# Optimization experiments

Hardware: AMD Instinct MI355X
Metric: run time of the kernel (lower is better)

## Reference

```python
import jax, jax.numpy as jnp
import numpy as np

B, S, DM, H, DK, R, THETA = 8, 2048, 512, 8, 64, 128, 10000.0
BLK = R          # key/query block size; window radius == block size
NB = S // BLK    # number of blocks
NEG = -1e30      # additive mask for invalid positions (fp32-safe)


def setup_inputs() -> dict:
    key = jax.random.key(0)
    ks = jax.random.split(key, 5)
    scale = 0.02
    hidden_states = jax.random.normal(ks[0], (B, S, DM), jnp.float32)
    Wq = jax.random.normal(ks[1], (DM, H * DK), jnp.float32) * scale
    Wk = jax.random.normal(ks[2], (DM, H * DK), jnp.float32) * scale
    Wv = jax.random.normal(ks[3], (DM, H * DK), jnp.float32) * scale
    Wo = jax.random.normal(ks[4], (H * DK, DM), jnp.float32) * scale
    position_ids = jnp.tile(jnp.arange(S, dtype=jnp.int64)[None, :], (B, 1))
    return {"hidden_states": hidden_states, "Wq": Wq, "Wk": Wk, "Wv": Wv,
            "Wo": Wo, "position_ids": position_ids}


def _apply_rope(q, k, position_ids):
    # q,k: [B,H,S,DK]; position_ids: [B,S]
    half = DK // 2
    inv_freq = 1.0 / (THETA ** (jnp.arange(0, DK, 2, dtype=jnp.float32) / DK))  # [half]
    freqs = position_ids.astype(jnp.float32)[:, :, None] * inv_freq[None, None, :]  # [B,S,half]
    emb = jnp.concatenate([freqs, freqs], axis=-1)        # [B,S,DK]
    cos = jnp.cos(emb)[:, None, :, :]                     # [B,1,S,DK]
    sin = jnp.sin(emb)[:, None, :, :]

    def rotate_half(x):
        return jnp.concatenate([-x[..., half:], x[..., :half]], axis=-1)

    return q * cos + rotate_half(q) * sin, k * cos + rotate_half(k) * sin


def _band_mask():
    # valid[nb, BLK, 3*BLK]: key within [0,S) and |j - i| <= R
    b = jnp.arange(NB)[:, None, None]
    qi = jnp.arange(BLK)[None, :, None]
    kj = jnp.arange(3 * BLK)[None, None, :]
    kglob = (b - 1) * BLK + kj                 # global key index
    qglob = b * BLK + qi                        # global query index
    return (jnp.abs(kglob - qglob) <= R) & (kglob >= 0) & (kglob < S)


def reference(hidden_states, Wq, Wk, Wv, Wo, position_ids):
    # projections: [B,S,DM] -> [B,H,S,DK]
    def shape(x):
        return x.reshape(B, S, H, DK).transpose(0, 2, 1, 3)

    q = shape(hidden_states @ Wq)
    k = shape(hidden_states @ Wk)
    v = shape(hidden_states @ Wv)
    q, k = _apply_rope(q, k, position_ids)

    # block-banded sliding-window attention, softmax_scale = 1.0 (no scaling)
    pad = ((0, 0), (0, 0), (BLK, BLK), (0, 0))
    kb = jnp.pad(k, pad).reshape(B, H, NB + 2, BLK, DK)
    vb = jnp.pad(v, pad).reshape(B, H, NB + 2, BLK, DK)
    # neighbor window: blocks [b-1, b, b+1] -> [B,H,NB,3*BLK,DK]
    kwin = jnp.concatenate([kb[:, :, i:i + NB] for i in range(3)], axis=3)
    vwin = jnp.concatenate([vb[:, :, i:i + NB] for i in range(3)], axis=3)
    qb = q.reshape(B, H, NB, BLK, DK)

    scores = jnp.einsum('bhnqd,bhnkd->bhnqk', qb, kwin)   # unscaled
    valid = _band_mask()                                  # [NB,BLK,3*BLK]
    scores = jnp.where(valid[None, None], scores, NEG)
    attn = jax.nn.softmax(scores.astype(jnp.float32), axis=-1).astype(scores.dtype)
    outb = jnp.einsum('bhnqk,bhnkd->bhnqd', attn, vwin)   # [B,H,NB,BLK,DK]

    out = outb.reshape(B, H, S, DK).transpose(0, 2, 1, 3).reshape(B, S, H * DK)
    return out @ Wo
```

## Files before the change

kernel.cpp:

```cpp
#include <hip/hip_runtime.h>

using bf16 = __bf16;
typedef __bf16 bf16x8 __attribute__((ext_vector_type(8)));
typedef __bf16 bf16x4 __attribute__((ext_vector_type(4)));
typedef float f32x4 __attribute__((ext_vector_type(4)));
typedef float f32x16 __attribute__((ext_vector_type(16)));

#define MFMA16(a, b, c) __builtin_amdgcn_mfma_f32_16x16x32_bf16((a), (b), (c), 0, 0, 0)
#define MFMA32(a, b, c) __builtin_amdgcn_mfma_f32_32x32x16_bf16((a), (b), (c), 0, 0, 0)

constexpr int S = 2048, DM = 512, H = 8, DK = 64, HD = 512;
constexpr int NBLK = 16, BLK = 128;
constexpr int Mrows = 8 * S;
constexpr float LOG2E = 1.44269504088896340736f;

__device__ __forceinline__ void gll16(const void* g, void* l) {
  __builtin_amdgcn_global_load_lds((const __attribute__((address_space(1))) unsigned int*)g,
                                   (__attribute__((address_space(3))) unsigned int*)l, 16, 0, 0);
}

__global__ void k_conv(const float* __restrict__ x, bf16* __restrict__ y) {
  size_t i = ((size_t)blockIdx.x * 256 + threadIdx.x) * 8;
  float4 a = *(const float4*)(x + i);
  float4 b = *(const float4*)(x + i + 4);
  bf16x8 o;
  o[0] = (bf16)a.x; o[1] = (bf16)a.y; o[2] = (bf16)a.z; o[3] = (bf16)a.w;
  o[4] = (bf16)b.x; o[5] = (bf16)b.y; o[6] = (bf16)b.z; o[7] = (bf16)b.w;
  *(bf16x8*)(y + i) = o;
}

__global__ void k_transw4(const float* __restrict__ W0, const float* __restrict__ W1,
                          const float* __restrict__ W2, const float* __restrict__ W3,
                          bf16* __restrict__ D0, bf16* __restrict__ D1,
                          bf16* __restrict__ D2, bf16* __restrict__ D3) {
  const int z = blockIdx.z;
  const float* W = (z == 0) ? W0 : (z == 1) ? W1 : (z == 2) ? W2 : W3;
  bf16* Wt = (z == 0) ? D0 : (z == 1) ? D1 : (z == 2) ? D2 : D3;
  __shared__ float tile[32][33];
  int k0 = blockIdx.x * 32, n0 = blockIdx.y * 32;
  int tx = threadIdx.x, ty = threadIdx.y;
#pragma unroll
  for (int i = 0; i < 4; i++)
    tile[ty * 4 + i][tx] = W[(size_t)(k0 + ty * 4 + i) * 512 + n0 + tx];
  __syncthreads();
#pragma unroll
  for (int i = 0; i < 4; i++)
    Wt[(size_t)(n0 + ty * 4 + i) * 512 + k0 + tx] = (bf16)tile[tx][ty * 4 + i];
}

__global__ void k_ctab(float2* __restrict__ ctab) {
  int idx = blockIdx.x * 256 + threadIdx.x;
  int s = idx >> 5, i = idx & 31;
  float invf = exp2f(-(float)i * (13.287712379549449f / 32.0f));
  float ang = (float)s * invf;
  ctab[idx] = make_float2(cosf(ang), sinf(ang));
}

__global__ __launch_bounds__(256) void k_gemm_qkv(
    const bf16* __restrict__ Xb,
    const bf16* __restrict__ Wtq, const bf16* __restrict__ Wtk, const bf16* __restrict__ Wtv,
    bf16* __restrict__ Qo, bf16* __restrict__ Ko, bf16* __restrict__ Vt,
    const float2* __restrict__ ctab) {
  const int bid = blockIdx.x;
  const int xcd = bid & 7, i = bid >> 3;
  const int mloc = i / 12, zy = i % 12;
  const int z = zy >> 2, y = zy & 3;
  const bf16* Wt = (z == 0) ? Wtq : ((z == 1) ? Wtk : Wtv);
  bf16* dst = (z == 0) ? Qo : Ko;
  const float qscale = (z == 0) ? LOG2E : 1.0f;

  __shared__ __align__(16) char Asm3[3][8192];
  __shared__ __align__(16) char Bsm3[3][8192];

  const int t = threadIdx.x, l = t & 63, wid = t >> 6;
  const int l15 = l & 15, l4 = l >> 4;
  const int wm = wid >> 1, wn = wid & 1;
  const size_t arow0 = (size_t)(xcd * 16 + mloc) * 128;
  const size_t brow0 = (size_t)y * 128;

  f32x4 acc[4][4] = {};
  const int rs = wid * 16 + (l >> 2);
  const int cs = (l & 3) ^ (l >> 4);

  auto stage = [&](int kt, int b) {
    const int k0 = kt * 32;
    gll16(Xb + (arow0 + rs) * 512 + k0 + cs * 8,      Asm3[b] + wid * 1024);
    gll16(Xb + (arow0 + 64 + rs) * 512 + k0 + cs * 8, Asm3[b] + 4096 + wid * 1024);
    gll16(Wt + (brow0 + rs) * 512 + k0 + cs * 8,      Bsm3[b] + wid * 1024);
    gll16(Wt + (brow0 + 64 + rs) * 512 + k0 + cs * 8, Bsm3[b] + 4096 + wid * 1024);
  };

  stage(0, 0);
  stage(1, 1);
  asm volatile("s_waitcnt vmcnt(4)" ::: "memory");
  __builtin_amdgcn_s_barrier();

  int cur = 0;
  for (int kt = 0; kt < 16; ++kt) {
    if (kt + 2 <= 15) stage(kt + 2, (kt + 2) % 3);
    bf16x8 af[4], bfr[4];
#pragma unroll
    for (int mi = 0; mi < 4; mi++) {
      int row = wm * 64 + mi * 16 + l15;
      af[mi] = *(const bf16x8*)(Asm3[cur] + row * 64 + ((l4 ^ (l15 >> 2)) * 16));
    }
#pragma unroll
    for (int ni = 0; ni < 4; ni++) {
      int row = wn * 64 + ni * 16 + l15;
      bfr[ni] = *(const bf16x8*)(Bsm3[cur] + row * 64 + ((l4 ^ (l15 >> 2)) * 16));
    }
#pragma unroll
    for (int mi = 0; mi < 4; mi++)
#pragma unroll
      for (int ni = 0; ni < 4; ni++)
        acc[mi][ni] = MFMA16(af[mi], bfr[ni], acc[mi][ni]);
    if (kt < 15) {
      if (kt < 14) asm volatile("s_waitcnt vmcnt(4)" ::: "memory");
      else         asm volatile("s_waitcnt vmcnt(0)" ::: "memory");
      __builtin_amdgcn_s_barrier();
    }
    cur = (cur == 2) ? 0 : cur + 1;
  }

  if (z == 2) {
    const int b = (int)(arow0 >> 11);
#pragma unroll
    for (int mi = 0; mi < 4; mi++) {
      int scol = (int)(arow0 & 2047) + wm * 64 + mi * 16 + l4 * 4;
#pragma unroll
      for (int ni = 0; ni < 4; ni++) {
        int col = (int)brow0 + wn * 64 + ni * 16 + l15;
        int hh = col >> 6, dd = col & 63;
        bf16x4 pk = {(bf16)acc[mi][ni][0], (bf16)acc[mi][ni][1],
                     (bf16)acc[mi][ni][2], (bf16)acc[mi][ni][3]};
        *(bf16x4*)(Vt + ((size_t)((b * H + hh) * 64 + dd)) * 2048 + scol) = pk;
      }
    }
    return;
  }

#pragma unroll
  for (int mi = 0; mi < 4; mi++) {
#pragma unroll
    for (int r = 0; r < 4; r++) {
      int grow = (int)arow0 + wm * 64 + mi * 16 + l4 * 4 + r;
      size_t rowoff = (size_t)grow * 512 + brow0 + wn * 64;
      int s = grow & (S - 1);
      float2 cs0 = ctab[s * 32 + l15];
      float2 cs1 = ctab[s * 32 + 16 + l15];
#pragma unroll
      for (int ni = 0; ni < 4; ni++) {
        float a = acc[mi][ni][r];
        float b = acc[mi][ni ^ 2][r];
        float2 cc = (ni & 1) ? cs1 : cs0;
        float val = (ni < 2) ? (a * cc.x - b * cc.y) : (a * cc.x + b * cc.y);
        dst[rowoff + ni * 16 + l15] = (bf16)(val * qscale);
      }
    }
  }
}

__global__ __launch_bounds__(256) void k_gemm_out(
    const bf16* __restrict__ A, const bf16* __restrict__ Wt, float* __restrict__ out) {
  const int bid = blockIdx.x;
  const int xcd = bid & 7, i = bid >> 3;
  __shared__ __align__(16) char Asm3[3][8192];
  __shared__ __align__(16) char Bsm3[3][8192];

  const int t = threadIdx.x, l = t & 63, wid = t >> 6;
  const int l15 = l & 15, l4 = l >> 4;
  const int wm = wid >> 1, wn = wid & 1;
  const size_t arow0 = (size_t)(xcd * 16 + (i >> 2)) * 128;
  const size_t brow0 = (size_t)(i & 3) * 128;

  f32x4 acc[4][4] = {};
  const int rs = wid * 16 + (l >> 2);
  const int cs = (l & 3) ^ (l >> 4);

  auto stage = [&](int kt, int b) {
    const int k0 = kt * 32;
    gll16(A + (arow0 + rs) * 512 + k0 + cs * 8,       Asm3[b] + wid * 1024);
    gll16(A + (arow0 + 64 + rs) * 512 + k0 + cs * 8,  Asm3[b] + 4096 + wid * 1024);
    gll16(Wt + (brow0 + rs) * 512 + k0 + cs * 8,      Bsm3[b] + wid * 1024);
    gll16(Wt + (brow0 + 64 + rs) * 512 + k0 + cs * 8, Bsm3[b] + 4096 + wid * 1024);
  };

  stage(0, 0);
  stage(1, 1);
  asm volatile("s_waitcnt vmcnt(4)" ::: "memory");
  __builtin_amdgcn_s_barrier();

  int cur = 0;
  for (int kt = 0; kt < 16; ++kt) {
    if (kt + 2 <= 15) stage(kt + 2, (kt + 2) % 3);
    bf16x8 af[4], bfr[4];
#pragma unroll
    for (int mi = 0; mi < 4; mi++) {
      int row = wm * 64 + mi * 16 + l15;
      af[mi] = *(const bf16x8*)(Asm3[cur] + row * 64 + ((l4 ^ (l15 >> 2)) * 16));
    }
#pragma unroll
    for (int ni = 0; ni < 4; ni++) {
      int row = wn * 64 + ni * 16 + l15;
      bfr[ni] = *(const bf16x8*)(Bsm3[cur] + row * 64 + ((l4 ^ (l15 >> 2)) * 16));
    }
#pragma unroll
    for (int mi = 0; mi < 4; mi++)
#pragma unroll
      for (int ni = 0; ni < 4; ni++)
        acc[mi][ni] = MFMA16(af[mi], bfr[ni], acc[mi][ni]);
    if (kt < 15) {
      if (kt < 14) asm volatile("s_waitcnt vmcnt(4)" ::: "memory");
      else         asm volatile("s_waitcnt vmcnt(0)" ::: "memory");
      __builtin_amdgcn_s_barrier();
    }
    cur = (cur == 2) ? 0 : cur + 1;
  }

#pragma unroll
  for (int mi = 0; mi < 4; mi++)
#pragma unroll
    for (int r = 0; r < 4; r++) {
      int grow = (int)arow0 + wm * 64 + mi * 16 + l4 * 4 + r;
      size_t rowoff = (size_t)grow * 512 + brow0 + wn * 64;
#pragma unroll
      for (int ni = 0; ni < 4; ni++)
        out[rowoff + ni * 16 + l15] = acc[mi][ni][r];
    }
}

__global__ __launch_bounds__(256, 4) void k_attn(
    const bf16* __restrict__ Q, const bf16* __restrict__ K, const bf16* __restrict__ Vt,
    bf16* __restrict__ O) {
  const int bid = blockIdx.x;
  const int swz = (bid & 7) * 128 + (bid >> 3);
  const int nb = swz & 15, h = (swz >> 4) & 7, bb = swz >> 7;
  const int t = threadIdx.x, l = t & 63, w = t >> 6;
  const int q31 = l & 31, hi = l >> 5;

  const int bh = bb * H + h;
  const size_t qrow = (size_t)bb * S + nb * BLK + w * 32 + q31;

  const bf16* Qp = Q + qrow * HD + h * DK + hi * 8;
  bf16x8 qb[4];
#pragma unroll
  for (int ks = 0; ks < 4; ks++) qb[ks] = *(const bf16x8*)(Qp + ks * 16);

  f32x16 o0 = {}, o1 = {};
  float mrun = -3e38f, lrun = 0.f;

  const bf16* Kbase = K + (size_t)bb * S * HD + h * DK + hi * 8;
  const bf16* Vbase = Vt + ((size_t)bh * 64 + q31) * 2048 + hi * 8;
  const int s0 = nb * BLK + w * 32 - 128;

  auto pv = [&](const f32x16& p, int kgc) {
    unsigned int Wd[4][2];
#pragma unroll
    for (int a = 0; a < 4; a++)
#pragma unroll
      for (int b2 = 0; b2 < 2; b2++) {
        unsigned int wd;
        asm("v_cvt_pk_bf16_f32 %0, %1, %2" : "=v"(wd) : "v"(p[4 * a + 2 * b2]), "v"(p[4 * a + 2 * b2 + 1]));
        Wd[a][b2] = wd;
      }
    bf16x8 pf[2];
#pragma unroll
    for (int ks = 0; ks < 2; ks++) {
      union { unsigned int u[4]; bf16x8 v; } cvt;
#pragma unroll
      for (int b2 = 0; b2 < 2; b2++) {
        unsigned int low_w = Wd[2 * ks][b2];
        unsigned int hi_w  = Wd[2 * ks + 1][b2];
        unsigned int msg = hi ? low_w : hi_w;
        unsigned int rec = __shfl_xor(msg, 32);
        cvt.u[b2]     = hi ? rec : low_w;
        cvt.u[2 + b2] = hi ? hi_w : rec;
      }
      pf[ks] = cvt.v;
    }
    const bf16* Vp = Vbase + kgc;
    __builtin_amdgcn_s_setprio(1);
    o0 = MFMA32(*(const bf16x8*)(Vp), pf[0], o0);
    o0 = MFMA32(*(const bf16x8*)(Vp + 16), pf[1], o0);
    o1 = MFMA32(*(const bf16x8*)(Vp + 32 * 2048), pf[0], o1);
    o1 = MFMA32(*(const bf16x8*)(Vp + 32 * 2048 + 16), pf[1], o1);
    __builtin_amdgcn_s_setprio(0);
  };

#pragma unroll
  for (int st = 0; st < 5; ++st) {
    const bool has2 = (st < 4);
    const int c0 = st * 2, c1 = c0 + 1;
    const int kg0 = s0 + c0 * 32, kg1 = s0 + c1 * 32;
    const int kc0 = kg0 < 0 ? 0 : (kg0 > S - 32 ? S - 32 : kg0);
    const int kc1 = kg1 < 0 ? 0 : (kg1 > S - 32 ? S - 32 : kg1);

    f32x16 a0 = {}, a1 = {};
    {
      const bf16* Kp = Kbase + (size_t)(kc0 + q31) * HD;
      __builtin_amdgcn_s_setprio(1);
      a0 = MFMA32(*(const bf16x8*)(Kp),      qb[0], a0);
      a0 = MFMA32(*(const bf16x8*)(Kp + 16), qb[1], a0);
      a0 = MFMA32(*(const bf16x8*)(Kp + 32), qb[2], a0);
      a0 = MFMA32(*(const bf16x8*)(Kp + 48), qb[3], a0);
      __builtin_amdgcn_s_setprio(0);
    }
    if (has2) {
      const bf16* Kp = Kbase + (size_t)(kc1 + q31) * HD;
      __builtin_amdgcn_s_setprio(1);
      a1 = MFMA32(*(const bf16x8*)(Kp),      qb[0], a1);
      a1 = MFMA32(*(const bf16x8*)(Kp + 16), qb[1], a1);
      a1 = MFMA32(*(const bf16x8*)(Kp + 32), qb[2], a1);
      a1 = MFMA32(*(const bf16x8*)(Kp + 48), qb[3], a1);
      __builtin_amdgcn_s_setprio(0);
    }

    if (kg0 != kc0) {
#pragma unroll
      for (int rg = 0; rg < 16; rg++) a0[rg] = -1e30f;
    } else if (c0 == 0) {
#pragma unroll
      for (int rg = 0; rg < 16; rg++) {
        int kk = (rg & 3) + 8 * (rg >> 2) + 4 * hi;
        if (kk < q31) a0[rg] = -1e30f;
      }
    } else if (c0 == 8) {
#pragma unroll
      for (int rg = 0; rg < 16; rg++) {
        int kk = (rg & 3) + 8 * (rg >> 2) + 4 * hi;
        if (kk > q31) a0[rg] = -1e30f;
      }
    }
    if (has2 && kg1 != kc1) {
#pragma unroll
      for (int rg = 0; rg < 16; rg++) a1[rg] = -1e30f;
    }

    f32x16 mx = a0;
    if (has2) {
#pragma unroll
      for (int rg = 0; rg < 16; rg++) mx[rg] = fmaxf(mx[rg], a1[rg]);
    }
#pragma unroll
    for (int sl = 8; sl >= 1; sl >>= 1)
#pragma unroll
      for (int i2 = 0; i2 < sl; i2++) mx[i2] = fmaxf(mx[i2], mx[i2 + sl]);
    const float pm = fmaxf(mx[0], __shfl_xor(mx[0], 32));

    if (!__all(pm - mrun <= 8.0f)) {
      const float mnew = fmaxf(mrun, pm);
      const float alpha = exp2f(mrun - mnew);
      lrun *= alpha;
#pragma unroll
      for (int rg = 0; rg < 16; rg++) { o0[rg] *= alpha; o1[rg] *= alpha; }
      mrun = mnew;
    }

    float rsum = 0.f;
#pragma unroll
    for (int rg = 0; rg < 16; rg++) { a0[rg] = exp2f(a0[rg] - mrun); rsum += a0[rg]; }
    if (has2) {
#pragma unroll
      for (int rg = 0; rg < 16; rg++) { a1[rg] = exp2f(a1[rg] - mrun); rsum += a1[rg]; }
    }
    rsum += __shfl_xor(rsum, 32);
    lrun += rsum;

    pv(a0, kc0);
    if (has2) pv(a1, kc1);
  }

  const float inv = 1.0f / lrun;
  bf16* Op = O + qrow * HD + h * DK + 4 * hi;
#pragma unroll
  for (int dt = 0; dt < 2; dt++) {
    const f32x16 oo = dt ? o1 : o0;
#pragma unroll
    for (int a = 0; a < 4; a++) {
      bf16x4 ob = {(bf16)(oo[4 * a + 0] * inv), (bf16)(oo[4 * a + 1] * inv),
                   (bf16)(oo[4 * a + 2] * inv), (bf16)(oo[4 * a + 3] * inv)};
      *(bf16x4*)(Op + dt * 32 + 8 * a) = ob;
    }
  }
}

extern "C" void kernel_launch(void* const* d_in, const int* in_sizes, int n_in,
                              void* d_out, int out_size, void* d_ws, size_t ws_size,
                              hipStream_t stream) {
  const float* hs = (const float*)d_in[0];
  const float* Wq = (const float*)d_in[1];
  const float* Wk = (const float*)d_in[2];
  const float* Wv = (const float*)d_in[3];
  const float* Wo = (const float*)d_in[4];
  float* out = (float*)d_out;

  char* ws = (char*)d_ws;
  const size_t MB = 1u << 20;
  bf16* Xb = (bf16*)(ws);
  bf16* Qb = (bf16*)(ws + 16 * MB);
  bf16* Kb = (bf16*)(ws + 32 * MB);
  bf16* Vt = (bf16*)(ws + 48 * MB);
  bf16* Wtq = (bf16*)(ws + 64 * MB);
  bf16* Wtk = Wtq + 512 * 512;
  bf16* Wtv = Wtk + 512 * 512;
  bf16* Wto = Wtv + 512 * 512;
  float2* ctab = (float2*)(ws + 64 * MB + 4 * 512 * 512 * sizeof(bf16));
  bf16* AO = Xb;

  k_conv<<<dim3(Mrows * DM / (256 * 8)), dim3(256), 0, stream>>>(hs, Xb);
  k_transw4<<<dim3(16, 16, 4), dim3(32, 8), 0, stream>>>(Wq, Wk, Wv, Wo, Wtq, Wtk, Wtv, Wto);
  k_ctab<<<dim3(S * 32 / 256), dim3(256), 0, stream>>>(ctab);
  k_gemm_qkv<<<dim3(1536), dim3(256), 0, stream>>>(Xb, Wtq, Wtk, Wtv, Qb, Kb, Vt, ctab);
  k_attn<<<dim3(NBLK * H * 8), dim3(256), 0, stream>>>(Qb, Kb, Vt, AO);
  k_gemm_out<<<dim3(512), dim3(256), 0, stream>>>(AO, Wto, out);
}
```

Before: 119.8 us.

## Repack K and V into 16-wide tiled layouts and retune LDS swizzle

The QKV projection epilogue now writes K as [bh][dchunk][s][16] and V as [bh][sgroup][d][16] tiles. The attention kernel reads these contiguous per-head slabs instead of strided rows of the full 512-wide K matrix and the 2048-wide transposed V. This is meant to improve global-memory coalescing and cache-line use for the K and V fragment loads in attention. The LDS XOR swizzle in both GEMMs also switches to a different lane-bit pattern to reduce bank conflicts. The attention kernel's address math and the GEMM epilogue stores are coupled, so both must match exactly.

```diff
diff --git a/kernel.cpp b/kernel.cpp
--- a/kernel.cpp
+++ b/kernel.cpp
@@ -66,7 +66,6 @@
   const int mloc = i / 12, zy = i % 12;
   const int z = zy >> 2, y = zy & 3;
   const bf16* Wt = (z == 0) ? Wtq : ((z == 1) ? Wtk : Wtv);
-  bf16* dst = (z == 0) ? Qo : Ko;
   const float qscale = (z == 0) ? LOG2E : 1.0f;
 
   __shared__ __align__(16) char Asm3[3][8192];
@@ -80,7 +79,7 @@
 
   f32x4 acc[4][4] = {};
   const int rs = wid * 16 + (l >> 2);
-  const int cs = (l & 3) ^ (l >> 4);
+  const int cs = (l & 3) ^ ((l >> 3) & 3);
 
   auto stage = [&](int kt, int b) {
     const int k0 = kt * 32;
@@ -102,12 +101,12 @@
 #pragma unroll
     for (int mi = 0; mi < 4; mi++) {
       int row = wm * 64 + mi * 16 + l15;
-      af[mi] = *(const bf16x8*)(Asm3[cur] + row * 64 + ((l4 ^ (l15 >> 2)) * 16));
+      af[mi] = *(const bf16x8*)(Asm3[cur] + row * 64 + ((l4 ^ ((l15 >> 1) & 3)) * 16));
     }
 #pragma unroll
     for (int ni = 0; ni < 4; ni++) {
       int row = wn * 64 + ni * 16 + l15;
-      bfr[ni] = *(const bf16x8*)(Bsm3[cur] + row * 64 + ((l4 ^ (l15 >> 2)) * 16));
+      bfr[ni] = *(const bf16x8*)(Bsm3[cur] + row * 64 + ((l4 ^ ((l15 >> 1) & 3)) * 16));
     }
 #pragma unroll
     for (int mi = 0; mi < 4; mi++)
@@ -122,18 +121,21 @@
     cur = (cur == 2) ? 0 : cur + 1;
   }
 
+  const int b = (int)(arow0 >> 11);
+  const int hh = (int)(brow0 >> 6) + wn;
+
   if (z == 2) {
-    const int b = (int)(arow0 >> 11);
+    const int sbase = (int)(arow0 & 2047) + wm * 64;
 #pragma unroll
     for (int mi = 0; mi < 4; mi++) {
-      int scol = (int)(arow0 & 2047) + wm * 64 + mi * 16 + l4 * 4;
+      int sg = (sbase + mi * 16) >> 4;
+      int slo = l4 * 4;
 #pragma unroll
       for (int ni = 0; ni < 4; ni++) {
-        int col = (int)brow0 + wn * 64 + ni * 16 + l15;
-        int hh = col >> 6, dd = col & 63;
+        int dd = ni * 16 + l15;
         bf16x4 pk = {(bf16)acc[mi][ni][0], (bf16)acc[mi][ni][1],
                      (bf16)acc[mi][ni][2], (bf16)acc[mi][ni][3]};
-        *(bf16x4*)(Vt + ((size_t)((b * H + hh) * 64 + dd)) * 2048 + scol) = pk;
+        *(bf16x4*)(Vt + (((size_t)(b * H + hh) * 128 + sg) * 64 + dd) * 16 + slo) = pk;
       }
     }
     return;
@@ -144,17 +146,20 @@
 #pragma unroll
     for (int r = 0; r < 4; r++) {
       int grow = (int)arow0 + wm * 64 + mi * 16 + l4 * 4 + r;
-      size_t rowoff = (size_t)grow * 512 + brow0 + wn * 64;
       int s = grow & (S - 1);
       float2 cs0 = ctab[s * 32 + l15];
       float2 cs1 = ctab[s * 32 + 16 + l15];
 #pragma unroll
       for (int ni = 0; ni < 4; ni++) {
         float a = acc[mi][ni][r];
-        float b = acc[mi][ni ^ 2][r];
+        float b2 = acc[mi][ni ^ 2][r];
         float2 cc = (ni & 1) ? cs1 : cs0;
-        float val = (ni < 2) ? (a * cc.x - b * cc.y) : (a * cc.x + b * cc.y);
-        dst[rowoff + ni * 16 + l15] = (bf16)(val * qscale);
+        float val = (ni < 2) ? (a * cc.x - b2 * cc.y) : (a * cc.x + b2 * cc.y);
+        if (z == 0) {
+          Qo[(size_t)grow * 512 + brow0 + wn * 64 + ni * 16 + l15] = (bf16)(val * qscale);
+        } else {
+          Ko[(((size_t)(b * H + hh) * 4 + ni) * 2048 + s) * 16 + l15] = (bf16)val;
+        }
       }
     }
   }
@@ -175,7 +180,7 @@
 
   f32x4 acc[4][4] = {};
   const int rs = wid * 16 + (l >> 2);
-  const int cs = (l & 3) ^ (l >> 4);
+  const int cs = (l & 3) ^ ((l >> 3) & 3);
 
   auto stage = [&](int kt, int b) {
     const int k0 = kt * 32;
@@ -197,12 +202,12 @@
 #pragma unroll
     for (int mi = 0; mi < 4; mi++) {
       int row = wm * 64 + mi * 16 + l15;
-      af[mi] = *(const bf16x8*)(Asm3[cur] + row * 64 + ((l4 ^ (l15 >> 2)) * 16));
+      af[mi] = *(const bf16x8*)(Asm3[cur] + row * 64 + ((l4 ^ ((l15 >> 1) & 3)) * 16));
     }
 #pragma unroll
     for (int ni = 0; ni < 4; ni++) {
       int row = wn * 64 + ni * 16 + l15;
-      bfr[ni] = *(const bf16x8*)(Bsm3[cur] + row * 64 + ((l4 ^ (l15 >> 2)) * 16));
+      bfr[ni] = *(const bf16x8*)(Bsm3[cur] + row * 64 + ((l4 ^ ((l15 >> 1) & 3)) * 16));
     }
 #pragma unroll
     for (int mi = 0; mi < 4; mi++)
@@ -230,7 +235,7 @@
 }
 
 __global__ __launch_bounds__(256, 4) void k_attn(
-    const bf16* __restrict__ Q, const bf16* __restrict__ K, const bf16* __restrict__ Vt,
+    const bf16* __restrict__ Q, const bf16* __restrict__ Kp, const bf16* __restrict__ VtP,
     bf16* __restrict__ O) {
   const int bid = blockIdx.x;
   const int swz = (bid & 7) * 128 + (bid >> 3);
@@ -249,8 +254,8 @@
   f32x16 o0 = {}, o1 = {};
   float mrun = -3e38f, lrun = 0.f;
 
-  const bf16* Kbase = K + (size_t)bb * S * HD + h * DK + hi * 8;
-  const bf16* Vbase = Vt + ((size_t)bh * 64 + q31) * 2048 + hi * 8;
+  const bf16* Kbh = Kp + (size_t)bh * 131072;
+  const bf16* Vbh = VtP + (size_t)bh * 131072;
   const int s0 = nb * BLK + w * 32 - 128;
 
   auto pv = [&](const f32x16& p, int kgc) {
@@ -278,12 +283,12 @@
       }
       pf[ks] = cvt.v;
     }
-    const bf16* Vp = Vbase + kgc;
+    const bf16* Vs = Vbh + (size_t)(kgc >> 4) * 1024 + q31 * 16 + hi * 8;
     __builtin_amdgcn_s_setprio(1);
-    o0 = MFMA32(*(const bf16x8*)(Vp), pf[0], o0);
-    o0 = MFMA32(*(const bf16x8*)(Vp + 16), pf[1], o0);
-    o1 = MFMA32(*(const bf16x8*)(Vp + 32 * 2048), pf[0], o1);
-    o1 = MFMA32(*(const bf16x8*)(Vp + 32 * 2048 + 16), pf[1], o1);
+    o0 = MFMA32(*(const bf16x8*)(Vs),               pf[0], o0);
+    o0 = MFMA32(*(const bf16x8*)(Vs + 1024),        pf[1], o0);
+    o1 = MFMA32(*(const bf16x8*)(Vs + 512),         pf[0], o1);
+    o1 = MFMA32(*(const bf16x8*)(Vs + 1024 + 512),  pf[1], o1);
     __builtin_amdgcn_s_setprio(0);
   };
 
@@ -297,21 +302,21 @@
 
     f32x16 a0 = {}, a1 = {};
     {
-      const bf16* Kp = Kbase + (size_t)(kc0 + q31) * HD;
+      const bf16* Kl = Kbh + (size_t)(kc0 + q31) * 16 + hi * 8;
       __builtin_amdgcn_s_setprio(1);
-      a0 = MFMA32(*(const bf16x8*)(Kp),      qb[0], a0);
-      a0 = MFMA32(*(const bf16x8*)(Kp + 16), qb[1], a0);
-      a0 = MFMA32(*(const bf16x8*)(Kp + 32), qb[2], a0);
-      a0 = MFMA32(*(const bf16x8*)(Kp + 48), qb[3], a0);
+      a0 = MFMA32(*(const bf16x8*)(Kl),          qb[0], a0);
+      a0 = MFMA32(*(const bf16x8*)(Kl + 32768),  qb[1], a0);
+      a0 = MFMA32(*(const bf16x8*)(Kl + 65536),  qb[2], a0);
+      a0 = MFMA32(*(const bf16x8*)(Kl + 98304),  qb[3], a0);
       __builtin_amdgcn_s_setprio(0);
     }
     if (has2) {
-      const bf16* Kp = Kbase + (size_t)(kc1 + q31) * HD;
+      const bf16* Kl = Kbh + (size_t)(kc1 + q31) * 16 + hi * 8;
       __builtin_amdgcn_s_setprio(1);
-      a1 = MFMA32(*(const bf16x8*)(Kp),      qb[0], a1);
-      a1 = MFMA32(*(const bf16x8*)(Kp + 16), qb[1], a1);
-      a1 = MFMA32(*(const bf16x8*)(Kp + 32), qb[2], a1);
-      a1 = MFMA32(*(const bf16x8*)(Kp + 48), qb[3], a1);
+      a1 = MFMA32(*(const bf16x8*)(Kl),          qb[0], a1);
+      a1 = MFMA32(*(const bf16x8*)(Kl + 32768),  qb[1], a1);
+      a1 = MFMA32(*(const bf16x8*)(Kl + 65536),  qb[2], a1);
+      a1 = MFMA32(*(const bf16x8*)(Kl + 98304),  qb[3], a1);
       __builtin_amdgcn_s_setprio(0);
     }
 
```

Result: faster. 110.3 us (-7.9%).
